# Optimization experiments

Hardware: AMD Instinct MI355X
Metric: run time of the kernel (lower is better)

The kernel has to match this reference:

```python
import jax, jax.numpy as jnp
import numpy as np

N_A, N_B = 100_000, 50_000
D, OUT = 128, 128
E = 1_000_000


def setup_inputs() -> dict:
    key = jax.random.key(0)
    ks = jax.random.split(key, 11)
    w_scale = np.sqrt(2.0 / (D + OUT)).astype(np.float32)  # glorot-ish
    return dict(
        x_a=jax.random.normal(ks[0], (N_A, D), dtype=jnp.float32),
        x_b=jax.random.normal(ks[1], (N_B, D), dtype=jnp.float32),
        W_ab=jax.random.normal(ks[2], (D, OUT), dtype=jnp.float32) * w_scale,
        W_ba=jax.random.normal(ks[3], (D, OUT), dtype=jnp.float32) * w_scale,
        W_aa=jax.random.normal(ks[4], (D, OUT), dtype=jnp.float32) * w_scale,
        src_ab=jax.random.randint(ks[5], (E,), 0, N_A, dtype=jnp.int32),
        dst_ab=jax.random.randint(ks[6], (E,), 0, N_B, dtype=jnp.int32),
        src_ba=jax.random.randint(ks[7], (E,), 0, N_B, dtype=jnp.int32),
        dst_ba=jax.random.randint(ks[8], (E,), 0, N_A, dtype=jnp.int32),
        src_aa=jax.random.randint(ks[9], (E,), 0, N_A, dtype=jnp.int32),
        dst_aa=jax.random.randint(ks[10], (E,), 0, N_A, dtype=jnp.int32),
    )


def _conv(x_src, W, src, dst, n_dst):
    """One edge type: source linear -> gather -> symmetric degree norm -> scatter-add."""
    n_src = x_src.shape[0]
    ones = jnp.ones(src.shape[0], dtype=x_src.dtype)
    deg_s = jax.ops.segment_sum(ones, src, num_segments=n_src)   # [n_src]
    deg_t = jax.ops.segment_sum(ones, dst, num_segments=n_dst)   # [n_dst]
    # every edge endpoint has degree >= 1, so the epsilon branch in the
    # original never affects the gathered norms
    norm = jnp.sqrt(deg_s[src] * deg_t[dst])                     # [E]
    msg = (x_src @ W)[src] / norm[:, None]                       # [E, OUT]
    return jax.ops.segment_sum(msg, dst, num_segments=n_dst)     # [n_dst, OUT]


def reference(x_a, x_b, W_ab, W_ba, W_aa,
              src_ab, dst_ab, src_ba, dst_ba, src_aa, dst_aa):
    # edge types: a->b, b->a, a->a; div['b'] = 1, div['a'] = 2
    out_b = _conv(x_a, W_ab, src_ab, dst_ab, x_b.shape[0])
    out_a = (_conv(x_b, W_ba, src_ba, dst_ba, x_a.shape[0])
             + _conv(x_a, W_aa, src_aa, dst_aa, x_a.shape[0])) * 0.5
    # original applies .relu() in the div step and again when ReLU=True (idempotent)
    return jax.nn.relu(out_a), jax.nn.relu(out_b)
```

## Files before the change

### kernel.cpp

```cpp
#include <hip/hip_runtime.h>


typedef __attribute__((ext_vector_type(8))) short short8;
typedef __attribute__((ext_vector_type(4))) float f32x4;

#define NB1 128

__device__ __forceinline__ ushort f2bf(float f) {
    uint u = __float_as_uint(f);
    return (ushort)((u + 0x7fffu + ((u >> 16) & 1u)) >> 16);
}
__device__ __forceinline__ float bflo(uint u) { return __uint_as_float(u << 16); }
__device__ __forceinline__ float bfhi(uint u) { return __uint_as_float(u & 0xffff0000u); }

struct SplitArgs {
    const int* key[6];
    const int* pay[3];
    uint2* rec2[3];
    uint* rec1[3];
    int E[6];
    uint M[6];
};

struct BuildArgs {
    const uint2* rec2[3];
    const uint* rec1[3];
    int E[6];
    int BW[6];
    int BINS[6];
    int* rp[3];
    int* pk[3];
    int* degS[3];
};

__global__ __launch_bounds__(256) void wt3_kernel(const float* __restrict__ W0,
                                                  const float* __restrict__ W1,
                                                  const float* __restrict__ W2,
                                                  ushort* __restrict__ T0,
                                                  ushort* __restrict__ T1,
                                                  ushort* __restrict__ T2) {
    const int idx = blockIdx.x * 256 + threadIdx.x;
    const int which = idx >> 14;
    const int j = idx & 16383;
    const float* W = (which == 0) ? W0 : (which == 1) ? W1 : W2;
    ushort* T = (which == 0) ? T0 : (which == 1) ? T1 : T2;
    const int n = j >> 7, k = j & 127;
    T[j] = f2bf(W[k * 128 + n]);
}

__global__ __launch_bounds__(256) void split_count_kernel(SplitArgs a,
                                                          int* __restrict__ counts) {
    const int r = blockIdx.x >> 7;
    const int bb = blockIdx.x & (NB1 - 1);
    const int E = a.E[r];
    const uint M = a.M[r];
    const int* key = a.key[r];
    __shared__ uint cnt[256];
    cnt[threadIdx.x] = 0;
    __syncthreads();
    const int C = (E + NB1 - 1) / NB1;
    const int lo = bb * C, hi = min(lo + C, E);
    for (int i = lo + threadIdx.x; i < hi; i += 256) {
        const uint b = (uint)(((unsigned long long)(uint)key[i] * M) >> 32);
        atomicAdd(&cnt[b], 1u);
    }
    __syncthreads();
    counts[(size_t)r * 32768 + threadIdx.x * NB1 + bb] = (int)cnt[threadIdx.x];
}

__global__ __launch_bounds__(256) void scan6_kernel(int* __restrict__ counts) {
    __shared__ int lds[256];
    __shared__ int carrySh;
    int* seg = counts + (size_t)blockIdx.x * 32768;
    int carry = 0;
    const int t = threadIdx.x;
    for (int round = 0; round < 32; ++round) {
        int4 v = *(int4*)&seg[round * 1024 + t * 4];
        const int lsum = v.x + v.y + v.z + v.w;
        lds[t] = lsum;
        __syncthreads();
        int acc = lsum;
        for (int off = 1; off < 256; off <<= 1) {
            const int o = (t >= off) ? lds[t - off] : 0;
            __syncthreads();
            acc += o;
            lds[t] = acc;
            __syncthreads();
        }
        const int base = carry + acc - lsum;
        int4 w;
        w.x = base;
        w.y = base + v.x;
        w.z = w.y + v.y;
        w.w = w.z + v.z;
        *(int4*)&seg[round * 1024 + t * 4] = w;
        if (t == 255) carrySh = acc;
        __syncthreads();
        carry += carrySh;
        __syncthreads();
    }
}

__global__ __launch_bounds__(256) void split_scatter_kernel(SplitArgs a,
                                                            const int* __restrict__ off) {
    const int r = blockIdx.x >> 7;
    const int bb = blockIdx.x & (NB1 - 1);
    const int E = a.E[r];
    const uint M = a.M[r];
    const int* key = a.key[r];
    __shared__ uint cur[256];
    cur[threadIdx.x] = (uint)off[(size_t)r * 32768 + threadIdx.x * NB1 + bb];
    __syncthreads();
    const int C = (E + NB1 - 1) / NB1;
    const int lo = bb * C, hi = min(lo + C, E);
    if (r < 3) {
        const int* pay = a.pay[r];
        uint2* rec = a.rec2[r];
        for (int i = lo + threadIdx.x; i < hi; i += 256) {
            const uint k = (uint)key[i];
            const uint b = (uint)(((unsigned long long)k * M) >> 32);
            const uint pos = atomicAdd(&cur[b], 1u);
            rec[pos] = make_uint2(k, (uint)pay[i]);
        }
    } else {
        uint* rec = a.rec1[r - 3];
        for (int i = lo + threadIdx.x; i < hi; i += 256) {
            const uint k = (uint)key[i];
            const uint b = (uint)(((unsigned long long)k * M) >> 32);
            const uint pos = atomicAdd(&cur[b], 1u);
            rec[pos] = k;
        }
    }
}

__global__ __launch_bounds__(256) void bucket_build_kernel(BuildArgs a,
                                                           const int* __restrict__ off) {
    const int r = blockIdx.x >> 8;
    const int bk = blockIdx.x & 255;
    const int E = a.E[r];
    const int BW = a.BW[r];
    const int BINS = a.BINS[r];
    const int start = off[(size_t)r * 32768 + bk * NB1];
    const int end = (bk < 255) ? off[(size_t)r * 32768 + (bk + 1) * NB1] : E;
    int n = end - start;
    const int binBase = bk * BW;
    const int W = min(BW, BINS - binBase);
    const int t = threadIdx.x;

    __shared__ uint hist[512];
    __shared__ uint hexc[512];
    __shared__ uint stmp[256];
    __shared__ ushort rank[16384];
    hist[t] = 0;
    hist[t + 256] = 0;
    __syncthreads();
    if (n > 16384) n = 16384;

    if (r < 3) {
        const uint2* rec = a.rec2[r] + start;
        for (int i = t; i < n; i += 256) {
            const int ld = (int)rec[i].x - binBase;
            rank[i] = (ushort)atomicAdd(&hist[ld], 1u);
        }
        __syncthreads();
        const uint va = hist[2 * t], vb = hist[2 * t + 1];
        const uint s = va + vb;
        stmp[t] = s;
        __syncthreads();
        uint acc = s;
        for (int o = 1; o < 256; o <<= 1) {
            const uint other = (t >= o) ? stmp[t - o] : 0;
            __syncthreads();
            acc += other;
            stmp[t] = acc;
            __syncthreads();
        }
        const uint ex = acc - s;
        hexc[2 * t] = ex;
        hexc[2 * t + 1] = ex + va;
        __syncthreads();
        int* rp = a.rp[r];
        for (int j = t; j < W; j += 256) rp[binBase + j] = start + (int)hexc[j];
        int* pk = a.pk[r];
        for (int i = t; i < n; i += 256) {
            const uint2 rc = rec[i];
            const int ld = (int)rc.x - binBase;
            pk[start + (int)hexc[ld] + (int)rank[i]] = (int)rc.y;
        }
    } else {
        const uint* rec = a.rec1[r - 3] + start;
        for (int i = t; i < n; i += 256)
            atomicAdd(&hist[(int)rec[i] - binBase], 1u);
        __syncthreads();
        int* dS = a.degS[r - 3];
        for (int j = t; j < W; j += 256) dS[binBase + j] = (int)hist[j];
    }
}

__global__ __launch_bounds__(256) void gemm_bf16(const float* __restrict__ X,
                                                 const ushort* __restrict__ Wt,
                                                 ushort* __restrict__ H, int M) {
    __shared__ ushort xs[128 * 128];
    __shared__ ushort wt[128 * 128];
    const int t = threadIdx.x;
    const int r0 = blockIdx.x * 128;

#pragma unroll
    for (int i = 0; i < 8; ++i) {
        const int idx = t + i * 256;
        const int row = idx >> 4;
        const int u = idx & 15;
        const int so = row * 128 + ((u ^ (row & 7)) << 3);
        short8 hx = {0, 0, 0, 0, 0, 0, 0, 0};
        if (r0 + row < M) {
            const float* sp = &X[(size_t)(r0 + row) * 128 + u * 8];
            const float4 f0 = *(const float4*)sp;
            const float4 f1 = *(const float4*)(sp + 4);
            hx[0] = (short)f2bf(f0.x); hx[1] = (short)f2bf(f0.y);
            hx[2] = (short)f2bf(f0.z); hx[3] = (short)f2bf(f0.w);
            hx[4] = (short)f2bf(f1.x); hx[5] = (short)f2bf(f1.y);
            hx[6] = (short)f2bf(f1.z); hx[7] = (short)f2bf(f1.w);
        }
        *(short8*)&xs[so] = hx;
        *(short8*)&wt[so] = *(const short8*)&Wt[row * 128 + u * 8];
    }
    __syncthreads();

    const int lane = t & 63;
    const int lr = lane & 15, lu = lane >> 4;
    const int wv = t >> 6;
    const int mbase = (wv >> 1) * 64;
    const int nbase = (wv & 1) * 64;

    f32x4 acc[4][4];
#pragma unroll
    for (int i = 0; i < 4; ++i)
#pragma unroll
        for (int j = 0; j < 4; ++j) acc[i][j] = (f32x4){0.f, 0.f, 0.f, 0.f};

#pragma unroll
    for (int kk = 0; kk < 4; ++kk) {
        const int u = kk * 4 + lu;
        short8 af[4], bf[4];
#pragma unroll
        for (int mt = 0; mt < 4; ++mt) {
            const int row = mbase + mt * 16 + lr;
            af[mt] = *(const short8*)&xs[row * 128 + ((u ^ (row & 7)) << 3)];
        }
#pragma unroll
        for (int nt = 0; nt < 4; ++nt) {
            const int row = nbase + nt * 16 + lr;
            bf[nt] = *(const short8*)&wt[row * 128 + ((u ^ (row & 7)) << 3)];
        }
#pragma unroll
        for (int mt = 0; mt < 4; ++mt)
#pragma unroll
            for (int nt = 0; nt < 4; ++nt)
                acc[mt][nt] = __builtin_amdgcn_mfma_f32_16x16x32_bf16(
                    af[mt], bf[nt], acc[mt][nt], 0, 0, 0);
    }

#pragma unroll
    for (int mt = 0; mt < 4; ++mt)
#pragma unroll
        for (int j = 0; j < 4; ++j) {
            const int grow = r0 + mbase + mt * 16 + lu * 4 + j;
            if (grow < M) {
#pragma unroll
                for (int nt = 0; nt < 4; ++nt)
                    H[(size_t)grow * 128 + nbase + nt * 16 + lr] =
                        f2bf(acc[mt][nt][j]);
            }
        }
}

__device__ __forceinline__ void csr_acc(const ushort* __restrict__ H,
                                        const int* __restrict__ pack,
                                        const int* __restrict__ degS,
                                        int start, int end, float dT, int c,
                                        float& a0, float& a1) {
    int j = start;
    for (; j + 4 <= end; j += 4) {
        const int s0 = pack[j], s1 = pack[j + 1], s2 = pack[j + 2], s3 = pack[j + 3];
        const uint v0 = *(const uint*)&H[(size_t)s0 * 128 + c];
        const uint v1 = *(const uint*)&H[(size_t)s1 * 128 + c];
        const uint v2 = *(const uint*)&H[(size_t)s2 * 128 + c];
        const uint v3 = *(const uint*)&H[(size_t)s3 * 128 + c];
        const float i0 = __frsqrt_rn((float)degS[s0] * dT);
        const float i1 = __frsqrt_rn((float)degS[s1] * dT);
        const float i2 = __frsqrt_rn((float)degS[s2] * dT);
        const float i3 = __frsqrt_rn((float)degS[s3] * dT);
        a0 = fmaf(bflo(v0), i0, a0); a1 = fmaf(bfhi(v0), i0, a1);
        a0 = fmaf(bflo(v1), i1, a0); a1 = fmaf(bfhi(v1), i1, a1);
        a0 = fmaf(bflo(v2), i2, a0); a1 = fmaf(bfhi(v2), i2, a1);
        a0 = fmaf(bflo(v3), i3, a0); a1 = fmaf(bfhi(v3), i3, a1);
    }
    for (; j < end; ++j) {
        const int s = pack[j];
        const uint v = *(const uint*)&H[(size_t)s * 128 + c];
        const float iv = __frsqrt_rn((float)degS[s] * dT);
        a0 = fmaf(bflo(v), iv, a0); a1 = fmaf(bfhi(v), iv, a1);
    }
}

__global__ __launch_bounds__(256) void agg1_kernel(const ushort* __restrict__ H,
                                                   const int* __restrict__ rp,
                                                   const int* __restrict__ pack,
                                                   const int* __restrict__ degS,
                                                   float* __restrict__ out,
                                                   int n_dst, int E) {
    const int lane = threadIdx.x & 63;
    const int w = (blockIdx.x * blockDim.x + threadIdx.x) >> 6;
    if (w >= n_dst) return;
    const int start = rp[w];
    const int end = (w + 1 < n_dst) ? rp[w + 1] : E;
    const int c = lane * 2;
    float a0 = 0.f, a1 = 0.f;
    csr_acc(H, pack, degS, start, end, (float)(end - start), c, a0, a1);
    float* o = &out[(size_t)w * 128 + c];
    o[0] = fmaxf(a0, 0.f);
    o[1] = fmaxf(a1, 0.f);
}

__global__ __launch_bounds__(256) void aggA_kernel(
    const ushort* __restrict__ Hba, const int* __restrict__ rpba,
    const int* __restrict__ packba, const int* __restrict__ degSba, int Eba,
    const ushort* __restrict__ Haa, const int* __restrict__ rpaa,
    const int* __restrict__ packaa, const int* __restrict__ degSaa, int Eaa,
    float* __restrict__ out, int n_dst) {
    const int lane = threadIdx.x & 63;
    const int w = (blockIdx.x * blockDim.x + threadIdx.x) >> 6;
    if (w >= n_dst) return;
    const int c = lane * 2;
    float a0 = 0.f, a1 = 0.f;
    {
        const int start = rpba[w];
        const int end = (w + 1 < n_dst) ? rpba[w + 1] : Eba;
        csr_acc(Hba, packba, degSba, start, end, (float)(end - start), c, a0, a1);
    }
    {
        const int start = rpaa[w];
        const int end = (w + 1 < n_dst) ? rpaa[w + 1] : Eaa;
        csr_acc(Haa, packaa, degSaa, start, end, (float)(end - start), c, a0, a1);
    }
    float* o = &out[(size_t)w * 128 + c];
    o[0] = fmaxf(0.5f * a0, 0.f);
    o[1] = fmaxf(0.5f * a1, 0.f);
}

extern "C" void kernel_launch(void* const* d_in, const int* in_sizes, int n_in,
                              void* d_out, int out_size, void* d_ws, size_t ws_size,
                              hipStream_t stream) {
    const float* x_a  = (const float*)d_in[0];
    const float* x_b  = (const float*)d_in[1];
    const float* W_ab = (const float*)d_in[2];
    const float* W_ba = (const float*)d_in[3];
    const float* W_aa = (const float*)d_in[4];
    const int* src_ab = (const int*)d_in[5];
    const int* dst_ab = (const int*)d_in[6];
    const int* src_ba = (const int*)d_in[7];
    const int* dst_ba = (const int*)d_in[8];
    const int* src_aa = (const int*)d_in[9];
    const int* dst_aa = (const int*)d_in[10];

    const int NA  = in_sizes[0] / 128;
    const int NB  = in_sizes[1] / 128;
    const int Eab = in_sizes[5];
    const int Eba = in_sizes[7];
    const int Eaa = in_sizes[9];
    const int Emax = max(Eab, max(Eba, Eaa));

    float* out_a = (float*)d_out;
    float* out_b = out_a + (size_t)NA * 128;

    char* p = (char*)d_ws;
    auto alloc = [&](size_t bytes) -> char* {
        char* q = p;
        p += (bytes + 255) & ~(size_t)255;
        return q;
    };
    int* pk_ab    = (int*)alloc((size_t)Emax * 4);
    int* pk_ba    = (int*)alloc((size_t)Emax * 4);
    int* pk_aa    = (int*)alloc((size_t)Emax * 4);
    int* rp_ab    = (int*)alloc((size_t)NB * 4);
    int* rp_ba    = (int*)alloc((size_t)NA * 4);
    int* rp_aa    = (int*)alloc((size_t)NA * 4);
    int* degS_ab  = (int*)alloc((size_t)NA * 4);
    int* degS_ba  = (int*)alloc((size_t)NB * 4);
    int* degS_aa  = (int*)alloc((size_t)NA * 4);
    int* counts   = (int*)alloc((size_t)6 * 32768 * 4);
    ushort* Wt_ab = (ushort*)alloc(128 * 128 * 2);
    ushort* Wt_ba = (ushort*)alloc(128 * 128 * 2);
    ushort* Wt_aa = (ushort*)alloc(128 * 128 * 2);
    const size_t recBytes = (size_t)Emax * (3 * 8 + 3 * 4);
    const size_t hBytes = (size_t)(NA + NB) * 128 * 2;
    char* ubase = alloc(recBytes > hBytes ? recBytes : hBytes);
    ushort* h1 = (ushort*)ubase;
    ushort* h2 = h1 + (size_t)NA * 128;
    uint2* rec2_0 = (uint2*)ubase;
    uint2* rec2_1 = rec2_0 + Emax;
    uint2* rec2_2 = rec2_1 + Emax;
    uint* rec1_0 = (uint*)(rec2_2 + Emax);
    uint* rec1_1 = rec1_0 + Emax;
    uint* rec1_2 = rec1_1 + Emax;

    const int BWa = (NA + 255) / 256, BWb = (NB + 255) / 256;
    const uint Ma = (uint)((0x100000000ULL + BWa - 1) / BWa);
    const uint Mb = (uint)((0x100000000ULL + BWb - 1) / BWb);

    SplitArgs sa;
    sa.key[0] = dst_ab; sa.key[1] = dst_ba; sa.key[2] = dst_aa;
    sa.key[3] = src_ab; sa.key[4] = src_ba; sa.key[5] = src_aa;
    sa.pay[0] = src_ab; sa.pay[1] = src_ba; sa.pay[2] = src_aa;
    sa.rec2[0] = rec2_0; sa.rec2[1] = rec2_1; sa.rec2[2] = rec2_2;
    sa.rec1[0] = rec1_0; sa.rec1[1] = rec1_1; sa.rec1[2] = rec1_2;
    sa.E[0] = Eab; sa.E[1] = Eba; sa.E[2] = Eaa;
    sa.E[3] = Eab; sa.E[4] = Eba; sa.E[5] = Eaa;
    sa.M[0] = Mb; sa.M[1] = Ma; sa.M[2] = Ma;
    sa.M[3] = Ma; sa.M[4] = Mb; sa.M[5] = Ma;

    BuildArgs ba;
    ba.rec2[0] = rec2_0; ba.rec2[1] = rec2_1; ba.rec2[2] = rec2_2;
    ba.rec1[0] = rec1_0; ba.rec1[1] = rec1_1; ba.rec1[2] = rec1_2;
    for (int i = 0; i < 6; ++i) ba.E[i] = sa.E[i];
    ba.BW[0] = BWb; ba.BW[1] = BWa; ba.BW[2] = BWa;
    ba.BW[3] = BWa; ba.BW[4] = BWb; ba.BW[5] = BWa;
    ba.BINS[0] = NB; ba.BINS[1] = NA; ba.BINS[2] = NA;
    ba.BINS[3] = NA; ba.BINS[4] = NB; ba.BINS[5] = NA;
    ba.rp[0] = rp_ab; ba.rp[1] = rp_ba; ba.rp[2] = rp_aa;
    ba.pk[0] = pk_ab; ba.pk[1] = pk_ba; ba.pk[2] = pk_aa;
    ba.degS[0] = degS_ab; ba.degS[1] = degS_ba; ba.degS[2] = degS_aa;

    wt3_kernel<<<192, 256, 0, stream>>>(W_ab, W_ba, W_aa, Wt_ab, Wt_ba, Wt_aa);
    split_count_kernel<<<6 * NB1, 256, 0, stream>>>(sa, counts);
    scan6_kernel<<<6, 256, 0, stream>>>(counts);
    split_scatter_kernel<<<6 * NB1, 256, 0, stream>>>(sa, counts);
    bucket_build_kernel<<<6 * 256, 256, 0, stream>>>(ba, counts);

    gemm_bf16<<<(NA + 127) / 128, 256, 0, stream>>>(x_a, Wt_ab, h1, NA);
    agg1_kernel<<<(NB + 3) / 4, 256, 0, stream>>>(h1, rp_ab, pk_ab, degS_ab,
                                                  out_b, NB, Eab);
    gemm_bf16<<<(NB + 127) / 128, 256, 0, stream>>>(x_b, Wt_ba, h2, NB);
    gemm_bf16<<<(NA + 127) / 128, 256, 0, stream>>>(x_a, Wt_aa, h1, NA);

    aggA_kernel<<<(NA + 3) / 4, 256, 0, stream>>>(h2, rp_ba, pk_ba, degS_ba, Eba,
                                                  h1, rp_aa, pk_aa, degS_aa, Eaa,
                                                  out_a, NA);
}
```

Before: 467.5 us.

## Sort CSR neighbor lists and split aggregation across wave halves with wider loads

Adds a kernel that bitonic-sorts each destination's source-index list within a wavefront, for lists of 2 to 64 entries, so gathers from H hit rows in ascending order and may get better cache locality. The aggregation kernels now have each half of the wavefront handle alternate edges and read 4 bf16 columns per lane with 8-byte loads. The two halves are combined with a cross-half shuffle and written as float4. This trades an extra launch and a pass over all packed indices for fewer, wider gather instructions and more memory-level parallelism per row.

```diff
diff --git a/kernel.cpp b/kernel.cpp
--- a/kernel.cpp
+++ b/kernel.cpp
@@ -197,6 +197,40 @@
     }
 }
 
+__global__ __launch_bounds__(256) void sort3_kernel(
+    int* __restrict__ pk0, const int* __restrict__ rp0, int n0, int E0,
+    int* __restrict__ pk1, const int* __restrict__ rp1, int n1, int E1,
+    int* __restrict__ pk2, const int* __restrict__ rp2, int n2, int E2) {
+    const int lane = threadIdx.x & 63;
+    const int w = (blockIdx.x * blockDim.x + threadIdx.x) >> 6;
+    int* pk; const int* rp; int n, E, row;
+    if (w < n0) {
+        pk = pk0; rp = rp0; n = n0; E = E0; row = w;
+    } else if (w < n0 + n1) {
+        pk = pk1; rp = rp1; n = n1; E = E1; row = w - n0;
+    } else if (w < n0 + n1 + n2) {
+        pk = pk2; rp = rp2; n = n2; E = E2; row = w - n0 - n1;
+    } else {
+        return;
+    }
+    const int start = rp[row];
+    const int end = (row + 1 < n) ? rp[row + 1] : E;
+    const int deg = end - start;
+    if (deg <= 1 || deg > 64) return;
+    int v = (lane < deg) ? pk[start + lane] : 0x7fffffff;
+#pragma unroll
+    for (int k = 2; k <= 64; k <<= 1) {
+#pragma unroll
+        for (int j = k >> 1; j > 0; j >>= 1) {
+            const int p = __shfl_xor(v, j);
+            const bool up = ((lane & k) == 0) || (k == 64);
+            const bool lower = ((lane & j) == 0);
+            v = (lower == up) ? min(v, p) : max(v, p);
+        }
+    }
+    if (lane < deg) pk[start + lane] = v;
+}
+
 __global__ __launch_bounds__(256) void gemm_bf16(const float* __restrict__ X,
                                                  const ushort* __restrict__ Wt,
                                                  ushort* __restrict__ H, int M) {
@@ -274,32 +308,43 @@
         }
 }
 
-__device__ __forceinline__ void csr_acc(const ushort* __restrict__ H,
-                                        const int* __restrict__ pack,
-                                        const int* __restrict__ degS,
-                                        int start, int end, float dT, int c,
-                                        float& a0, float& a1) {
+__device__ __forceinline__ void csr_acc2(const ushort* __restrict__ H,
+                                         const int* __restrict__ pack,
+                                         const int* __restrict__ degS,
+                                         int start, int end, float dT,
+                                         int cl, int half, float* a) {
+    const int c = cl * 4;
     int j = start;
-    for (; j + 4 <= end; j += 4) {
-        const int s0 = pack[j], s1 = pack[j + 1], s2 = pack[j + 2], s3 = pack[j + 3];
-        const uint v0 = *(const uint*)&H[(size_t)s0 * 128 + c];
-        const uint v1 = *(const uint*)&H[(size_t)s1 * 128 + c];
-        const uint v2 = *(const uint*)&H[(size_t)s2 * 128 + c];
-        const uint v3 = *(const uint*)&H[(size_t)s3 * 128 + c];
-        const float i0 = __frsqrt_rn((float)degS[s0] * dT);
-        const float i1 = __frsqrt_rn((float)degS[s1] * dT);
-        const float i2 = __frsqrt_rn((float)degS[s2] * dT);
-        const float i3 = __frsqrt_rn((float)degS[s3] * dT);
-        a0 = fmaf(bflo(v0), i0, a0); a1 = fmaf(bfhi(v0), i0, a1);
-        a0 = fmaf(bflo(v1), i1, a0); a1 = fmaf(bfhi(v1), i1, a1);
-        a0 = fmaf(bflo(v2), i2, a0); a1 = fmaf(bfhi(v2), i2, a1);
-        a0 = fmaf(bflo(v3), i3, a0); a1 = fmaf(bfhi(v3), i3, a1);
-    }
-    for (; j < end; ++j) {
-        const int s = pack[j];
-        const uint v = *(const uint*)&H[(size_t)s * 128 + c];
-        const float iv = __frsqrt_rn((float)degS[s] * dT);
-        a0 = fmaf(bflo(v), iv, a0); a1 = fmaf(bfhi(v), iv, a1);
+    for (; j + 8 <= end; j += 8) {
+        int s[4];
+        float iv[4];
+        uint2 v[4];
+#pragma unroll
+        for (int p = 0; p < 4; ++p) {
+            s[p] = pack[j + 2 * p + half];
+            v[p] = *(const uint2*)&H[(size_t)s[p] * 128 + c];
+        }
+#pragma unroll
+        for (int p = 0; p < 4; ++p) iv[p] = __frsqrt_rn((float)degS[s[p]] * dT);
+#pragma unroll
+        for (int p = 0; p < 4; ++p) {
+            a[0] = fmaf(bflo(v[p].x), iv[p], a[0]);
+            a[1] = fmaf(bfhi(v[p].x), iv[p], a[1]);
+            a[2] = fmaf(bflo(v[p].y), iv[p], a[2]);
+            a[3] = fmaf(bfhi(v[p].y), iv[p], a[3]);
+        }
+    }
+    for (; j < end; j += 2) {
+        const int e = j + half;
+        const bool valid = e < end;
+        const int es = valid ? e : end - 1;
+        const int s = pack[es];
+        const uint2 v = *(const uint2*)&H[(size_t)s * 128 + c];
+        const float iv = valid ? __frsqrt_rn((float)degS[s] * dT) : 0.f;
+        a[0] = fmaf(bflo(v.x), iv, a[0]);
+        a[1] = fmaf(bfhi(v.x), iv, a[1]);
+        a[2] = fmaf(bflo(v.y), iv, a[2]);
+        a[3] = fmaf(bfhi(v.y), iv, a[3]);
     }
 }
 
@@ -314,12 +359,17 @@
     if (w >= n_dst) return;
     const int start = rp[w];
     const int end = (w + 1 < n_dst) ? rp[w + 1] : E;
-    const int c = lane * 2;
-    float a0 = 0.f, a1 = 0.f;
-    csr_acc(H, pack, degS, start, end, (float)(end - start), c, a0, a1);
-    float* o = &out[(size_t)w * 128 + c];
-    o[0] = fmaxf(a0, 0.f);
-    o[1] = fmaxf(a1, 0.f);
+    const int cl = lane & 31, half = lane >> 5;
+    float a[4] = {0.f, 0.f, 0.f, 0.f};
+    csr_acc2(H, pack, degS, start, end, (float)(end - start), cl, half, a);
+#pragma unroll
+    for (int i = 0; i < 4; ++i) a[i] += __shfl_xor(a[i], 32);
+    if (half == 0) {
+        float4 o;
+        o.x = fmaxf(a[0], 0.f); o.y = fmaxf(a[1], 0.f);
+        o.z = fmaxf(a[2], 0.f); o.w = fmaxf(a[3], 0.f);
+        *(float4*)&out[(size_t)w * 128 + cl * 4] = o;
+    }
 }
 
 __global__ __launch_bounds__(256) void aggA_kernel(
@@ -331,21 +381,26 @@
     const int lane = threadIdx.x & 63;
     const int w = (blockIdx.x * blockDim.x + threadIdx.x) >> 6;
     if (w >= n_dst) return;
-    const int c = lane * 2;
-    float a0 = 0.f, a1 = 0.f;
+    const int cl = lane & 31, half = lane >> 5;
+    float a[4] = {0.f, 0.f, 0.f, 0.f};
     {
         const int start = rpba[w];
         const int end = (w + 1 < n_dst) ? rpba[w + 1] : Eba;
-        csr_acc(Hba, packba, degSba, start, end, (float)(end - start), c, a0, a1);
+        csr_acc2(Hba, packba, degSba, start, end, (float)(end - start), cl, half, a);
     }
     {
         const int start = rpaa[w];
         const int end = (w + 1 < n_dst) ? rpaa[w + 1] : Eaa;
-        csr_acc(Haa, packaa, degSaa, start, end, (float)(end - start), c, a0, a1);
-    }
-    float* o = &out[(size_t)w * 128 + c];
-    o[0] = fmaxf(0.5f * a0, 0.f);
-    o[1] = fmaxf(0.5f * a1, 0.f);
+        csr_acc2(Haa, packaa, degSaa, start, end, (float)(end - start), cl, half, a);
+    }
+#pragma unroll
+    for (int i = 0; i < 4; ++i) a[i] += __shfl_xor(a[i], 32);
+    if (half == 0) {
+        float4 o;
+        o.x = fmaxf(0.5f * a[0], 0.f); o.y = fmaxf(0.5f * a[1], 0.f);
+        o.z = fmaxf(0.5f * a[2], 0.f); o.w = fmaxf(0.5f * a[3], 0.f);
+        *(float4*)&out[(size_t)w * 128 + cl * 4] = o;
+    }
 }
 
 extern "C" void kernel_launch(void* const* d_in, const int* in_sizes, int n_in,
@@ -437,6 +492,10 @@
     split_scatter_kernel<<<6 * NB1, 256, 0, stream>>>(sa, counts);
     bucket_build_kernel<<<6 * 256, 256, 0, stream>>>(ba, counts);
 
+    const int nrows = NB + NA + NA;
+    sort3_kernel<<<(nrows + 3) / 4, 256, 0, stream>>>(
+        pk_ab, rp_ab, NB, Eab, pk_ba, rp_ba, NA, Eba, pk_aa, rp_aa, NA, Eaa);
+
     gemm_bf16<<<(NA + 127) / 128, 256, 0, stream>>>(x_a, Wt_ab, h1, NA);
     agg1_kernel<<<(NB + 3) / 4, 256, 0, stream>>>(h1, rp_ab, pk_ab, degS_ab,
                                                   out_b, NB, Eab);
```

New measurement: 518.7 us. 10.9% more time.
